# Performance work log

Hardware: AMD Instinct MI355X
Metric: run time of the kernel (lower is better)

## Reference

```python
import jax, jax.numpy as jnp
import numpy as np

B, S, D, H, HS = 4, 2048, 1024, 16, 64
DFF = 4 * D
EPS = 1e-5


def setup_inputs() -> dict:
    key = jax.random.key(0)
    ks = jax.random.split(key, 16)
    std = 0.02
    return {
        "x": jax.random.normal(ks[0], (B, S, D), jnp.float32),
        "Wq": jax.random.normal(ks[1], (H, D, HS), jnp.float32) * std,
        "bq": jnp.zeros((H, HS), jnp.float32),
        "Wk": jax.random.normal(ks[2], (H, D, HS), jnp.float32) * std,
        "bk": jnp.zeros((H, HS), jnp.float32),
        "Wv": jax.random.normal(ks[3], (H, D, HS), jnp.float32) * std,
        "bv": jnp.zeros((H, HS), jnp.float32),
        "Wp": jax.random.normal(ks[4], (D, D), jnp.float32) * std,
        "bp": jnp.zeros((D,), jnp.float32),
        "ln1_w": jnp.ones((D,), jnp.float32),
        "ln1_b": jnp.zeros((D,), jnp.float32),
        "ln2_w": jnp.ones((D,), jnp.float32),
        "ln2_b": jnp.zeros((D,), jnp.float32),
        "W1": jax.random.normal(ks[5], (D, DFF), jnp.float32) * std,
        "b1": jnp.zeros((DFF,), jnp.float32),
        "W2": jax.random.normal(ks[6], (DFF, D), jnp.float32) * std,
        "b2": jnp.zeros((D,), jnp.float32),
    }


def _layernorm(x, w, b):
    mu = jnp.mean(x, axis=-1, keepdims=True)
    var = jnp.mean(jnp.square(x - mu), axis=-1, keepdims=True)
    return (x - mu) * jax.lax.rsqrt(var + EPS) * w + b


def _block(x, Wq, bq, Wk, bk, Wv, bv, Wp, bp, ln1_w, ln1_b, ln2_w, ln2_b, W1, b1, W2, b2):
    seq = x.shape[1]
    xn = _layernorm(x, ln1_w, ln1_b)
    # batched per-head projections: [B,H,S,HS]
    q = jnp.einsum('bsd,hdk->bhsk', xn, Wq) + bq[:, None, :]
    k = jnp.einsum('bsd,hdk->bhsk', xn, Wk) + bk[:, None, :]
    v = jnp.einsum('bsd,hdk->bhsk', xn, Wv) + bv[:, None, :]
    scores = jnp.einsum('bhsk,bhtk->bhst', q, k)
    mask = jnp.tril(jnp.ones((seq, seq), bool))
    # original: masked_fill(-inf) then divide by sqrt(head_size) -> equivalent
    scores = jnp.where(mask, scores / jnp.sqrt(jnp.float32(HS)), -jnp.inf)
    attn = jax.nn.softmax(scores, axis=-1)
    out = jnp.einsum('bhst,bhtk->bhsk', attn, v)
    out = out.transpose(0, 2, 1, 3).reshape(x.shape[0], seq, H * HS)
    att = out @ Wp + bp
    x = x + att
    xn2 = _layernorm(x, ln2_w, ln2_b)
    h = jax.nn.gelu(xn2 @ W1 + b1, approximate=False)  # torch nn.GELU default = exact
    ffn = h @ W2 + b2
    return x + ffn


def reference(x, Wq, bq, Wk, bk, Wv, bv, Wp, bp, ln1_w, ln1_b, ln2_w, ln2_b, W1, b1, W2, b2):
    out = _block(x, Wq, bq, Wk, bk, Wv, bv, Wp, bp, ln1_w, ln1_b, ln2_w, ln2_b, W1, b1, W2, b2)
    return out
```

## Files before the change

### kernel.cpp

```cpp
#include <hip/hip_runtime.h>
#include <hip/hip_bf16.h>

#define D_MODEL 1024
#define SEQ 2048
#define NH 16
#define HSZ 64
#define DFF_ 4096

typedef __attribute__((ext_vector_type(8))) short short8;
typedef __attribute__((ext_vector_type(4))) short short4v;
typedef __attribute__((ext_vector_type(4))) float f32x4;

static __device__ __forceinline__ short f2bf(float f) {
  unsigned u = __builtin_bit_cast(unsigned, f);
  u = u + 0x7fffu + ((u >> 16) & 1u);
  return (short)(u >> 16);
}

static __device__ __forceinline__ unsigned packbf2(float a, float b) {
  return (unsigned)(unsigned short)f2bf(a) | ((unsigned)(unsigned short)f2bf(b) << 16);
}

static __device__ __forceinline__ f32x4 mfma16(short8 a, short8 b, f32x4 c) {
  return __builtin_amdgcn_mfma_f32_16x16x32_bf16(a, b, c, 0, 0, 0);
}

static __device__ __forceinline__ void gld16(const short* g, short* l) {
  __builtin_amdgcn_global_load_lds((const __attribute__((address_space(1))) void*)g,
                                   (__attribute__((address_space(3))) void*)l, 16, 0, 0);
}

#define SM_SCALE 0.18033688011112042f
#define VMW(n) asm volatile("s_waitcnt vmcnt(" #n ")" ::: "memory")

__global__ void transpose_qkv_kernel(const float* __restrict__ Wq, const float* __restrict__ Wk,
                                     const float* __restrict__ Wv, short* __restrict__ dst) {
  __shared__ float tile[32][33];
  const int z = blockIdx.z;
  const int which = z >> 4, hh = z & 15;
  const float* src = (which == 0 ? Wq : which == 1 ? Wk : Wv) + (long)hh * (D_MODEL * HSZ);
  const int c0 = blockIdx.x * 32, r0 = blockIdx.y * 32;
  const int tx = threadIdx.x, ty = threadIdx.y;
#pragma unroll
  for (int i = 0; i < 4; ++i)
    tile[ty + 8 * i][tx] = src[(long)(r0 + ty + 8 * i) * HSZ + c0 + tx];
  __syncthreads();
#pragma unroll
  for (int i = 0; i < 4; ++i)
    dst[((long)which * 1024 + hh * 64 + c0 + ty + 8 * i) * D_MODEL + r0 + tx] =
        f2bf(tile[tx][ty + 8 * i]);
}

__global__ void transpose_gen_kernel(const float* __restrict__ src, short* __restrict__ dst,
                                     int R, int C) {
  __shared__ float tile[32][33];
  const int c0 = blockIdx.x * 32, r0 = blockIdx.y * 32;
  const int tx = threadIdx.x, ty = threadIdx.y;
#pragma unroll
  for (int i = 0; i < 4; ++i)
    tile[ty + 8 * i][tx] = src[(long)(r0 + ty + 8 * i) * C + c0 + tx];
  __syncthreads();
#pragma unroll
  for (int i = 0; i < 4; ++i)
    dst[(long)(c0 + ty + 8 * i) * R + r0 + tx] = f2bf(tile[tx][ty + 8 * i]);
}

__global__ void v_transpose_kernel(const short* __restrict__ vb, short* __restrict__ vt) {
  __shared__ short tile[64 * 72];
  const int bh = blockIdx.y;
  const int t0 = blockIdx.x * 64;
  const long base = (long)bh * SEQ * HSZ;
  const int tid = threadIdx.x;
  const int r = tid >> 3, c = (tid & 7) * 8;
#pragma unroll
  for (int it = 0; it < 2; ++it) {
    const int rr = r + it * 32;
    *(short8*)&tile[rr * 72 + c] = *(const short8*)(vb + base + (long)(t0 + rr) * HSZ + c);
  }
  __syncthreads();
#pragma unroll
  for (int it = 0; it < 2; ++it) {
    const int rr = r + it * 32;
    short8 o;
#pragma unroll
    for (int u = 0; u < 8; ++u) o[u] = tile[(c + u) * 72 + rr];
    *(short8*)(vt + base + (long)rr * SEQ + t0 + c) = o;
  }
}

__global__ void ln_kernel(const float* __restrict__ x, const float* __restrict__ w,
                          const float* __restrict__ b, short* __restrict__ out) {
  const int row = blockIdx.x;
  const float* xr = x + (size_t)row * D_MODEL;
  const int t = threadIdx.x;
  float4 v = *(const float4*)(xr + t * 4);
  float s = v.x + v.y + v.z + v.w;
  float s2 = v.x * v.x + v.y * v.y + v.z * v.z + v.w * v.w;
#pragma unroll
  for (int o = 1; o < 64; o <<= 1) {
    s += __shfl_xor(s, o, 64);
    s2 += __shfl_xor(s2, o, 64);
  }
  __shared__ float ps[8];
  const int lane = t & 63, wid = t >> 6;
  if (lane == 0) { ps[wid] = s; ps[wid + 4] = s2; }
  __syncthreads();
  s = ps[0] + ps[1] + ps[2] + ps[3];
  s2 = ps[4] + ps[5] + ps[6] + ps[7];
  const float mu = s * (1.0f / D_MODEL);
  const float var = s2 * (1.0f / D_MODEL) - mu * mu;
  const float rs = rsqrtf(var + 1e-5f);
  float4 wv = *(const float4*)(w + t * 4);
  float4 bv = *(const float4*)(b + t * 4);
  short4v o4;
  o4[0] = f2bf((v.x - mu) * rs * wv.x + bv.x);
  o4[1] = f2bf((v.y - mu) * rs * wv.y + bv.y);
  o4[2] = f2bf((v.z - mu) * rs * wv.z + bv.z);
  o4[3] = f2bf((v.w - mu) * rs * wv.w + bv.w);
  *(short4v*)(out + (size_t)row * D_MODEL + t * 4) = o4;
}

template <int MODE, int BM>
__global__ __launch_bounds__(512, 2) void gemm_kernel(
    const short* __restrict__ A, const short* __restrict__ Bt, const int K,
    const float* __restrict__ c0, const float* __restrict__ c1,
    const float* __restrict__ c2, const float* __restrict__ res,
    void* __restrict__ o0, void* __restrict__ o1, void* __restrict__ o2) {
  constexpr int NPH = BM / 64;
  constexpr int NA = BM / 64;
  constexpr int NTOT = NA + 4;
  constexpr int PER = NTOT / NPH;
  constexpr int HM = BM / 2;
  __shared__ short As[2][BM * 64];
  __shared__ short Bs[2][256 * 64];
  const long r0 = (long)blockIdx.y * BM;
  const long n0 = (long)blockIdx.x * 256;
  const int tid = threadIdx.x;
  const int lane = tid & 63, wid = tid >> 6;
  const int wm = wid >> 2, wn = wid & 3;
  const int l16 = lane & 15, lg = lane >> 4;

  long offA[NA], offB[4];
#pragma unroll
  for (int i = 0; i < NA; ++i) {
    const int c = tid + i * 512;
    const int lam = c >> 3, s = c & 7;
    const int cch = lam >> 6, rho = lam & 63;
    const int g = cch * 32 + (rho & 31) + ((rho >> 5) ? HM : 0);
    offA[i] = (long)(r0 + g) * K + ((s ^ (lam & 7)) << 3);
  }
#pragma unroll
  for (int i = 0; i < 4; ++i) {
    const int c = tid + i * 512;
    const int row = c >> 3, s = c & 7;
    offB[i] = (long)(n0 + row) * K + ((s ^ (row & 7)) << 3);
  }

  f32x4 acc[2 * NPH][4];
#pragma unroll
  for (int m = 0; m < 2 * NPH; ++m)
#pragma unroll
    for (int n = 0; n < 4; ++n) {
      f32x4 z = {0.f, 0.f, 0.f, 0.f};
      acc[m][n] = z;
    }

  const int x7 = l16 & 7;
  const int sw0 = (lg ^ x7) * 8, sw1 = ((4 + lg) ^ x7) * 8;

#define STG(j, kt, buf)                                                      \
  {                                                                          \
    if ((j) < 4)                                                             \
      gld16(Bt + offB[(j)] + (kt), &Bs[buf][(tid + (j)*512) * 8]);           \
    else                                                                     \
      gld16(A + offA[(j)-4] + (kt), &As[buf][(tid + ((j)-4) * 512) * 8]);    \
  }

#define GPHASE(P, ENDSTMT)                                                   \
  {                                                                          \
    short8 af[2][2];                                                         \
    _Pragma("unroll") for (int mm = 0; mm < 2; ++mm) {                       \
      const int lam = (P)*64 + wm * 32 + mm * 16 + l16;                      \
      af[mm][0] = *(const short8*)&Ap[lam * 64 + sw0];                       \
      af[mm][1] = *(const short8*)&Ap[lam * 64 + sw1];                       \
    }                                                                        \
    if ((P) == 0) {                                                          \
      _Pragma("unroll") for (int n = 0; n < 4; ++n) {                        \
        const int r = (wn * 64 + n * 16 + l16) * 64;                         \
        bf[n][0] = *(const short8*)&Bp[r + sw0];                             \
        bf[n][1] = *(const short8*)&Bp[r + sw1];                             \
      }                                                                      \
    }                                                                        \
    if (st) {                                                                \
      _Pragma("unroll") for (int j = (P)*PER; j < ((P) + 1) * PER; ++j)      \
          STG(j, ktn, nb);                                                   \
    }                                                                        \
    __builtin_amdgcn_s_barrier();                                            \
    asm volatile("s_waitcnt lgkmcnt(0)" ::: "memory");                       \
    __builtin_amdgcn_sched_barrier(0);                                       \
    __builtin_amdgcn_s_setprio(1);                                           \
    _Pragma("unroll") for (int kk = 0; kk < 2; ++kk)                         \
        _Pragma("unroll") for (int mm = 0; mm < 2; ++mm)                     \
        _Pragma("unroll") for (int n = 0; n < 4; ++n) acc[2 * (P) + mm][n] = \
        mfma16(af[mm][kk], bf[n][kk], acc[2 * (P) + mm][n]);                 \
    __builtin_amdgcn_s_setprio(0);                                           \
    ENDSTMT;                                                                 \
    __builtin_amdgcn_s_barrier();                                            \
  }

  const int NT = K >> 6;
#pragma unroll
  for (int j = 0; j < NTOT; ++j) STG(j, 0, 0);
  if constexpr (BM == 256) VMW(3); else VMW(1);
  __builtin_amdgcn_s_barrier();

  for (int t = 0; t < NT; ++t) {
    const int cur = t & 1, nb = cur ^ 1;
    const short* Ap = As[cur];
    const short* Bp = Bs[cur];
    const bool st = (t + 1 < NT);
    const int ktn = (t + 1) << 6;
    short8 bf[4][2];
    if constexpr (BM == 256) {
      GPHASE(0, { if (st) VMW(4); else VMW(2); });
      GPHASE(1, { if (st) VMW(5); else VMW(1); });
      GPHASE(2, { if (st) VMW(6); else VMW(0); });
      GPHASE(3, { if (st) VMW(3); });
    } else {
      GPHASE(0, { if (st) VMW(3); else VMW(0); });
      GPHASE(1, { if (st) VMW(1); });
    }
  }
#undef GPHASE
#undef STG

#pragma unroll
  for (int m = 0; m < 2 * NPH; ++m) {
    const long rowb = r0 + wm * HM + m * 16 + lg * 4;
#pragma unroll
    for (int n = 0; n < 4; ++n) {
      const long col = n0 + wn * 64 + n * 16 + l16;
#pragma unroll
      for (int j = 0; j < 4; ++j) {
        float val = acc[m][n][j];
        const long rr = rowb + j;
        if (MODE == 0) {
          const int c10 = (int)col & 1023;
          const int which = (int)col >> 10;
          const float* bb = which == 0 ? c0 : which == 1 ? c1 : c2;
          short* oo = (short*)(which == 0 ? o0 : which == 1 ? o1 : o2);
          val += bb[c10];
          if (which == 0) val *= SM_SCALE;
          const long bidx = rr >> 11, sidx = rr & 2047;
          const int h = c10 >> 6, hs = c10 & 63;
          oo[(((bidx * NH) + h) * SEQ + sidx) * HSZ + hs] = f2bf(val);
        } else if (MODE == 1) {
          val += c0[col] + res[rr * D_MODEL + col];
          ((float*)o0)[rr * D_MODEL + col] = val;
        } else if (MODE == 2) {
          val += c0[col];
          const float g = 0.5f * val * (1.0f + erff(val * 0.70710678118654752f));
          ((short*)o0)[rr * DFF_ + col] = f2bf(g);
        } else {
          val += c0[col] + res[rr * D_MODEL + col];
          ((float*)o0)[rr * D_MODEL + col] = val;
        }
      }
    }
  }
}

__global__ void attn_kernel(const short* __restrict__ q, const short* __restrict__ k,
                            const short* __restrict__ vt, short* __restrict__ att) {
  const int qt = (SEQ / 128 - 1) - (int)blockIdx.y;
  const int bh = blockIdx.x;
  const int b = bh >> 4, h = bh & 15;
  const int tid = threadIdx.x;
  const int lane = tid & 63, wq = tid >> 6;
  const int l16 = lane & 15, lg = lane >> 4;
  const long base = (long)bh * SEQ * HSZ;

  __shared__ short Ks[64 * 64];
  __shared__ short Vts[64 * 64];
  __shared__ short Ps[4 * 32 * 72];
  short* Psw = &Ps[wq * 32 * 72];

  const int R0 = qt * 128 + wq * 32;

  short8 qf[2][2];
#pragma unroll
  for (int qn = 0; qn < 2; ++qn)
#pragma unroll
    for (int kk = 0; kk < 2; ++kk)
      qf[qn][kk] =
          *(const short8*)(q + base + (long)(R0 + qn * 16 + l16) * HSZ + kk * 32 + lg * 8);

  float m_[2] = {-INFINITY, -INFINITY};
  float l_[2] = {0.f, 0.f};
  f32x4 oacc[2][4];
#pragma unroll
  for (int qn = 0; qn < 2; ++qn)
#pragma unroll
    for (int hf = 0; hf < 4; ++hf) {
      f32x4 z = {0.f, 0.f, 0.f, 0.f};
      oacc[qn][hf] = z;
    }

  const int srow = tid >> 3, wg = tid & 7;
  const int swc = (wg ^ (srow & 7)) * 8;
  const int x7 = l16 & 7;
  const int rc0 = (lg ^ x7) * 8, rc1 = ((4 + lg) ^ x7) * 8;
  const int tend = (qt + 1) * 128;

  for (int t0 = 0; t0 < tend; t0 += 64) {
    __syncthreads();
#pragma unroll
    for (int it = 0; it < 2; ++it) {
      const int r = srow + it * 32;
      const short8 kv = *(const short8*)(k + base + (long)(t0 + r) * HSZ + wg * 8);
      const short8 vv = *(const short8*)(vt + base + (long)r * SEQ + t0 + wg * 8);
      *(short8*)&Ks[r * 64 + swc] = kv;
      *(short8*)&Vts[r * 64 + swc] = vv;
    }
    __syncthreads();

    if (t0 <= R0 + 31) {
      f32x4 sf[4][2];
#pragma unroll
      for (int tt = 0; tt < 4; ++tt)
#pragma unroll
        for (int qn = 0; qn < 2; ++qn) {
          f32x4 z = {0.f, 0.f, 0.f, 0.f};
          sf[tt][qn] = z;
        }
      __builtin_amdgcn_s_setprio(1);
#pragma unroll
      for (int kk = 0; kk < 2; ++kk)
#pragma unroll
        for (int tt = 0; tt < 4; ++tt) {
          short8 kf = *(const short8*)&Ks[(tt * 16 + l16) * 64 + (kk ? rc1 : rc0)];
#pragma unroll
          for (int qn = 0; qn < 2; ++qn) sf[tt][qn] = mfma16(kf, qf[qn][kk], sf[tt][qn]);
        }
      __builtin_amdgcn_s_setprio(0);

      const bool domask = (t0 + 63 > R0);
      if (domask) {
        const int tb = t0 + lg * 4;
#pragma unroll
        for (int tt = 0; tt < 4; ++tt)
#pragma unroll
          for (int qn = 0; qn < 2; ++qn) {
            const int qg = R0 + qn * 16 + l16;
#pragma unroll
            for (int j = 0; j < 4; ++j)
              if (tb + tt * 16 + j > qg) sf[tt][qn][j] = -INFINITY;
          }
      }

      float mx[2];
#pragma unroll
      for (int qn = 0; qn < 2; ++qn) {
        float m0 = sf[0][qn][0];
#pragma unroll
        for (int tt = 0; tt < 4; ++tt)
#pragma unroll
          for (int j = 0; j < 4; ++j) m0 = fmaxf(m0, sf[tt][qn][j]);
        m0 = fmaxf(m0, __shfl_xor(m0, 16, 64));
        m0 = fmaxf(m0, __shfl_xor(m0, 32, 64));
        mx[qn] = m0;
      }
      const int ok = (mx[0] <= m_[0] + 8.f) && (mx[1] <= m_[1] + 8.f);
      if (!__all(ok)) {
#pragma unroll
        for (int qn = 0; qn < 2; ++qn) {
          const float mnew = fmaxf(m_[qn], mx[qn]);
          const float rc = exp2f(m_[qn] - mnew);
          m_[qn] = mnew;
          l_[qn] *= rc;
#pragma unroll
          for (int hf = 0; hf < 4; ++hf)
#pragma unroll
            for (int j = 0; j < 4; ++j) oacc[qn][hf][j] *= rc;
        }
      }
#pragma unroll
      for (int qn = 0; qn < 2; ++qn) {
        float sum = 0.f;
#pragma unroll
        for (int tt = 0; tt < 4; ++tt)
#pragma unroll
          for (int j = 0; j < 4; ++j) {
            const float p = exp2f(sf[tt][qn][j] - m_[qn]);
            sf[tt][qn][j] = p;
            sum += p;
          }
        l_[qn] += sum;
      }

#pragma unroll
      for (int qn = 0; qn < 2; ++qn)
#pragma unroll
        for (int tt = 0; tt < 4; ++tt) {
          const int ro = (qn * 16 + l16) * 72 + tt * 16 + lg * 4;
          *(unsigned*)&Psw[ro] = packbf2(sf[tt][qn][0], sf[tt][qn][1]);
          *(unsigned*)&Psw[ro + 2] = packbf2(sf[tt][qn][2], sf[tt][qn][3]);
        }

      __builtin_amdgcn_s_setprio(1);
#pragma unroll
      for (int kk = 0; kk < 2; ++kk) {
        short8 pa[2];
#pragma unroll
        for (int qn = 0; qn < 2; ++qn)
          pa[qn] = *(const short8*)&Psw[(qn * 16 + l16) * 72 + kk * 32 + lg * 8];
#pragma unroll
        for (int hf = 0; hf < 4; ++hf) {
          short8 vf = *(const short8*)&Vts[(hf * 16 + l16) * 64 + (kk ? rc1 : rc0)];
#pragma unroll
          for (int qn = 0; qn < 2; ++qn)
            oacc[qn][hf] = mfma16(vf, pa[qn], oacc[qn][hf]);
        }
      }
      __builtin_amdgcn_s_setprio(0);
    }
  }

#pragma unroll
  for (int qn = 0; qn < 2; ++qn) {
    float lt = l_[qn];
    lt += __shfl_xor(lt, 16, 64);
    lt += __shfl_xor(lt, 32, 64);
    const float inv = 1.0f / lt;
    const long row = R0 + qn * 16 + l16;
#pragma unroll
    for (int hf = 0; hf < 4; ++hf) {
      short4v o4;
#pragma unroll
      for (int j = 0; j < 4; ++j) o4[j] = f2bf(oacc[qn][hf][j] * inv);
      *(short4v*)(att + ((long)b * SEQ + row) * D_MODEL + h * HSZ + hf * 16 + lg * 4) = o4;
    }
  }
}

extern "C" void kernel_launch(void* const* d_in, const int* in_sizes, int n_in,
                              void* d_out, int out_size, void* d_ws, size_t ws_size,
                              hipStream_t stream) {
  const float* x = (const float*)d_in[0];
  const float* Wq = (const float*)d_in[1];
  const float* bq = (const float*)d_in[2];
  const float* Wk = (const float*)d_in[3];
  const float* bk = (const float*)d_in[4];
  const float* Wv = (const float*)d_in[5];
  const float* bv = (const float*)d_in[6];
  const float* Wp = (const float*)d_in[7];
  const float* bp = (const float*)d_in[8];
  const float* g1 = (const float*)d_in[9];
  const float* be1 = (const float*)d_in[10];
  const float* g2 = (const float*)d_in[11];
  const float* be2 = (const float*)d_in[12];
  const float* W1 = (const float*)d_in[13];
  const float* b1 = (const float*)d_in[14];
  const float* W2 = (const float*)d_in[15];
  const float* b2 = (const float*)d_in[16];
  float* out = (float*)d_out;
  char* ws = (char*)d_ws;

  if (ws_size < 209715200ull) return;

  short* WqkvT = (short*)(ws + 0);
  short* WpT = (short*)(ws + 6291456);
  short* W1T = (short*)(ws + 8388608);
  short* W2T = (short*)(ws + 16777216);
  short* xn = (short*)(ws + 25165824);
  short* vt = (short*)(ws + 25165824);
  short* qb = (short*)(ws + 41943040);
  short* kb = (short*)(ws + 58720256);
  short* vb = (short*)(ws + 75497472);
  short* att = (short*)(ws + 92274688);
  float* x1 = (float*)(ws + 109051904);
  short* hb = (short*)(ws + 142606336);

  dim3 tb(32, 8);
  transpose_qkv_kernel<<<dim3(2, 32, 48), tb, 0, stream>>>(Wq, Wk, Wv, WqkvT);
  transpose_gen_kernel<<<dim3(32, 32), tb, 0, stream>>>(Wp, WpT, 1024, 1024);
  transpose_gen_kernel<<<dim3(128, 32), tb, 0, stream>>>(W1, W1T, 1024, 4096);
  transpose_gen_kernel<<<dim3(32, 128), tb, 0, stream>>>(W2, W2T, 4096, 1024);
  ln_kernel<<<8192, 256, 0, stream>>>(x, g1, be1, xn);
  gemm_kernel<0, 128><<<dim3(12, 64), 512, 0, stream>>>(xn, WqkvT, 1024, bq, bk, bv,
                                                        nullptr, qb, kb, vb);
  v_transpose_kernel<<<dim3(32, 64), 256, 0, stream>>>(vb, vt);
  attn_kernel<<<dim3(64, 16), 256, 0, stream>>>(qb, kb, vt, att);
  gemm_kernel<1, 128><<<dim3(4, 64), 512, 0, stream>>>(att, WpT, 1024, bp, nullptr,
                                                       nullptr, x, x1, nullptr, nullptr);
  ln_kernel<<<8192, 256, 0, stream>>>(x1, g2, be2, xn);
  gemm_kernel<2, 256><<<dim3(16, 32), 512, 0, stream>>>(xn, W1T, 1024, b1, nullptr,
                                                        nullptr, nullptr, hb, nullptr,
                                                        nullptr);
  gemm_kernel<3, 128><<<dim3(4, 64), 512, 0, stream>>>(hb, W2T, 4096, b2, nullptr,
                                                       nullptr, x1, out, nullptr, nullptr);
}
```

Baseline: 414.8 us.

## Add dedicated 256x256 GEMM with 8-phase interleaved staging for QKV and FFN1

Adds a specialized 256x256-tile GEMM kernel that splits each pair of K-tiles into eight phases, each issuing a quarter of the next tile's global-to-LDS loads while running MFMAs, with finer-grained vmcnt waits. The QKV projection moves from 128-row tiles to 256-row tiles (halving grid rows), and the FFN up-projection uses the new kernel. The generic gemm kernel is trimmed to the 128-row residual modes. This aims to improve load/compute overlap and operand reuse; the 256x256 tile uses more LDS and registers, which may limit occupancy, and the smaller QKV grid may underfill the CUs.

```diff
diff --git a/kernel.cpp b/kernel.cpp
--- a/kernel.cpp
+++ b/kernel.cpp
@@ -118,6 +118,153 @@
   o4[2] = f2bf((v.z - mu) * rs * wv.z + bv.z);
   o4[3] = f2bf((v.w - mu) * rs * wv.w + bv.w);
   *(short4v*)(out + (size_t)row * D_MODEL + t * 4) = o4;
+}
+
+template <int MODE>
+__global__ __launch_bounds__(512, 2) void gemm256_kernel(
+    const short* __restrict__ A, const short* __restrict__ Bt, const int K,
+    const float* __restrict__ c0, const float* __restrict__ c1,
+    const float* __restrict__ c2, void* __restrict__ o0, void* __restrict__ o1,
+    void* __restrict__ o2) {
+  __shared__ short As[2][256 * 64];
+  __shared__ short Bs[2][256 * 64];
+  const long r0 = (long)blockIdx.y * 256;
+  const long n0 = (long)blockIdx.x * 256;
+  const int tid = threadIdx.x;
+  const int lane = tid & 63, wid = tid >> 6;
+  const int wm = wid >> 2, wn = wid & 3;
+  const int l16 = lane & 15, lg = lane >> 4;
+
+  long offA[4], offB[4];
+#pragma unroll
+  for (int i = 0; i < 4; ++i) {
+    const int c = tid + i * 512;
+    const int lam = c >> 3, s = c & 7;
+    const int cch = lam >> 6, rho = lam & 63;
+    const int g = cch * 32 + (rho & 31) + ((rho >> 5) ? 128 : 0);
+    offA[i] = (long)(r0 + g) * K + ((s ^ (lam & 7)) << 3);
+    offB[i] = (long)(n0 + lam) * K + ((s ^ (lam & 7)) << 3);
+  }
+
+  f32x4 acc[8][4];
+#pragma unroll
+  for (int m = 0; m < 8; ++m)
+#pragma unroll
+    for (int n = 0; n < 4; ++n) {
+      f32x4 z = {0.f, 0.f, 0.f, 0.f};
+      acc[m][n] = z;
+    }
+
+  const int x7 = l16 & 7;
+  const int sw0 = (lg ^ x7) * 8, sw1 = ((4 + lg) ^ x7) * 8;
+
+#define SA(T, buf, h)                                                          \
+  {                                                                            \
+    gld16(A + offA[2 * (h)] + ((T) << 6), &As[buf][(tid + (2 * (h)) * 512) * 8]); \
+    gld16(A + offA[2 * (h) + 1] + ((T) << 6),                                  \
+          &As[buf][(tid + (2 * (h) + 1) * 512) * 8]);                          \
+  }
+#define SB(T, buf, h)                                                          \
+  {                                                                            \
+    gld16(Bt + offB[2 * (h)] + ((T) << 6), &Bs[buf][(tid + (2 * (h)) * 512) * 8]); \
+    gld16(Bt + offB[2 * (h) + 1] + ((T) << 6),                                 \
+          &Bs[buf][(tid + (2 * (h) + 1) * 512) * 8]);                          \
+  }
+
+#define PH(P, STAGE, WAITST)                                                   \
+  {                                                                            \
+    const short* Ap = As[(P) < 4 ? 0 : 1];                                     \
+    const short* Bp = Bs[(P) < 4 ? 0 : 1];                                     \
+    short8 af[2][2];                                                           \
+    _Pragma("unroll") for (int mm = 0; mm < 2; ++mm) {                         \
+      const int lam = ((P) & 3) * 64 + wm * 32 + mm * 16 + l16;                \
+      af[mm][0] = *(const short8*)&Ap[lam * 64 + sw0];                         \
+      af[mm][1] = *(const short8*)&Ap[lam * 64 + sw1];                         \
+    }                                                                          \
+    if (((P) & 3) == 0) {                                                      \
+      _Pragma("unroll") for (int n = 0; n < 4; ++n) {                          \
+        const int r = (wn * 64 + n * 16 + l16) * 64;                           \
+        bf[n][0] = *(const short8*)&Bp[r + sw0];                               \
+        bf[n][1] = *(const short8*)&Bp[r + sw1];                               \
+      }                                                                        \
+    }                                                                          \
+    STAGE;                                                                     \
+    __builtin_amdgcn_s_barrier();                                              \
+    asm volatile("s_waitcnt lgkmcnt(0)" ::: "memory");                         \
+    __builtin_amdgcn_sched_barrier(0);                                         \
+    __builtin_amdgcn_s_setprio(1);                                             \
+    _Pragma("unroll") for (int kk = 0; kk < 2; ++kk)                           \
+        _Pragma("unroll") for (int mm = 0; mm < 2; ++mm)                       \
+        _Pragma("unroll") for (int n = 0; n < 4; ++n)                          \
+            acc[((P) & 3) * 2 + mm][n] =                                       \
+        mfma16(af[mm][kk], bf[n][kk], acc[((P) & 3) * 2 + mm][n]);             \
+    __builtin_amdgcn_s_setprio(0);                                             \
+    WAITST;                                                                    \
+    __builtin_amdgcn_s_barrier();                                              \
+  }
+
+  const int NT = K >> 6;
+  const int NI = NT >> 1;
+  SB(0, 0, 0); SB(0, 0, 1); SA(0, 0, 0); SA(0, 0, 1);
+  SB(1, 1, 0); SB(1, 1, 1); SA(1, 1, 0);
+  VMW(8);
+  __builtin_amdgcn_s_barrier();
+
+  for (int i = 0; i < NI; ++i) {
+    const int T0 = 2 * i, T1 = 2 * i + 1;
+    short8 bf[4][2];
+    if (i + 1 < NI) {
+      PH(0, SA(T1, 1, 1), ((void)0));
+      PH(1, SB(T0 + 2, 0, 0), VMW(10));
+      PH(2, SB(T0 + 2, 0, 1), ((void)0));
+      PH(3, SA(T0 + 2, 0, 0), VMW(8));
+      PH(4, SA(T0 + 2, 0, 1), ((void)0));
+      PH(5, SB(T1 + 2, 1, 0), VMW(10));
+      PH(6, SB(T1 + 2, 1, 1), ((void)0));
+      PH(7, SA(T1 + 2, 1, 0), VMW(8));
+    } else {
+      PH(0, SA(T1, 1, 1), VMW(0));
+      PH(1, ((void)0), ((void)0));
+      PH(2, ((void)0), ((void)0));
+      PH(3, ((void)0), ((void)0));
+      PH(4, ((void)0), ((void)0));
+      PH(5, ((void)0), ((void)0));
+      PH(6, ((void)0), ((void)0));
+      PH(7, ((void)0), ((void)0));
+    }
+  }
+#undef PH
+#undef SA
+#undef SB
+
+#pragma unroll
+  for (int m = 0; m < 8; ++m) {
+    const long rowb = r0 + wm * 128 + (m >> 1) * 32 + (m & 1) * 16 + lg * 4;
+#pragma unroll
+    for (int n = 0; n < 4; ++n) {
+      const long col = n0 + wn * 64 + n * 16 + l16;
+#pragma unroll
+      for (int j = 0; j < 4; ++j) {
+        float val = acc[m][n][j];
+        const long rr = rowb + j;
+        if (MODE == 0) {
+          const int c10 = (int)col & 1023;
+          const int which = (int)col >> 10;
+          const float* bb = which == 0 ? c0 : which == 1 ? c1 : c2;
+          short* oo = (short*)(which == 0 ? o0 : which == 1 ? o1 : o2);
+          val += bb[c10];
+          if (which == 0) val *= SM_SCALE;
+          const long bidx = rr >> 11, sidx = rr & 2047;
+          const int h = c10 >> 6, hs = c10 & 63;
+          oo[(((bidx * NH) + h) * SEQ + sidx) * HSZ + hs] = f2bf(val);
+        } else {
+          val += c0[col];
+          const float g = 0.5f * val * (1.0f + erff(val * 0.70710678118654752f));
+          ((short*)o0)[rr * DFF_ + col] = f2bf(g);
+        }
+      }
+    }
+  }
 }
 
 template <int MODE, int BM>
@@ -211,7 +358,7 @@
   const int NT = K >> 6;
 #pragma unroll
   for (int j = 0; j < NTOT; ++j) STG(j, 0, 0);
-  if constexpr (BM == 256) VMW(3); else VMW(1);
+  VMW(1);
   __builtin_amdgcn_s_barrier();
 
   for (int t = 0; t < NT; ++t) {
@@ -221,15 +368,8 @@
     const bool st = (t + 1 < NT);
     const int ktn = (t + 1) << 6;
     short8 bf[4][2];
-    if constexpr (BM == 256) {
-      GPHASE(0, { if (st) VMW(4); else VMW(2); });
-      GPHASE(1, { if (st) VMW(5); else VMW(1); });
-      GPHASE(2, { if (st) VMW(6); else VMW(0); });
-      GPHASE(3, { if (st) VMW(3); });
-    } else {
-      GPHASE(0, { if (st) VMW(3); else VMW(0); });
-      GPHASE(1, { if (st) VMW(1); });
-    }
+    GPHASE(0, { if (st) VMW(3); else VMW(0); });
+    GPHASE(1, { if (st) VMW(1); });
   }
 #undef GPHASE
 #undef STG
@@ -244,23 +384,9 @@
       for (int j = 0; j < 4; ++j) {
         float val = acc[m][n][j];
         const long rr = rowb + j;
-        if (MODE == 0) {
-          const int c10 = (int)col & 1023;
-          const int which = (int)col >> 10;
-          const float* bb = which == 0 ? c0 : which == 1 ? c1 : c2;
-          short* oo = (short*)(which == 0 ? o0 : which == 1 ? o1 : o2);
-          val += bb[c10];
-          if (which == 0) val *= SM_SCALE;
-          const long bidx = rr >> 11, sidx = rr & 2047;
-          const int h = c10 >> 6, hs = c10 & 63;
-          oo[(((bidx * NH) + h) * SEQ + sidx) * HSZ + hs] = f2bf(val);
-        } else if (MODE == 1) {
+        if (MODE == 1) {
           val += c0[col] + res[rr * D_MODEL + col];
           ((float*)o0)[rr * D_MODEL + col] = val;
-        } else if (MODE == 2) {
-          val += c0[col];
-          const float g = 0.5f * val * (1.0f + erff(val * 0.70710678118654752f));
-          ((short*)o0)[rr * DFF_ + col] = f2bf(g);
         } else {
           val += c0[col] + res[rr * D_MODEL + col];
           ((float*)o0)[rr * D_MODEL + col] = val;
@@ -487,16 +613,15 @@
   transpose_gen_kernel<<<dim3(128, 32), tb, 0, stream>>>(W1, W1T, 1024, 4096);
   transpose_gen_kernel<<<dim3(32, 128), tb, 0, stream>>>(W2, W2T, 4096, 1024);
   ln_kernel<<<8192, 256, 0, stream>>>(x, g1, be1, xn);
-  gemm_kernel<0, 128><<<dim3(12, 64), 512, 0, stream>>>(xn, WqkvT, 1024, bq, bk, bv,
-                                                        nullptr, qb, kb, vb);
+  gemm256_kernel<0><<<dim3(12, 32), 512, 0, stream>>>(xn, WqkvT, 1024, bq, bk, bv, qb,
+                                                      kb, vb);
   v_transpose_kernel<<<dim3(32, 64), 256, 0, stream>>>(vb, vt);
   attn_kernel<<<dim3(64, 16), 256, 0, stream>>>(qb, kb, vt, att);
   gemm_kernel<1, 128><<<dim3(4, 64), 512, 0, stream>>>(att, WpT, 1024, bp, nullptr,
                                                        nullptr, x, x1, nullptr, nullptr);
   ln_kernel<<<8192, 256, 0, stream>>>(x1, g2, be2, xn);
-  gemm_kernel<2, 256><<<dim3(16, 32), 512, 0, stream>>>(xn, W1T, 1024, b1, nullptr,
-                                                        nullptr, nullptr, hb, nullptr,
-                                                        nullptr);
+  gemm256_kernel<2><<<dim3(16, 32), 512, 0, stream>>>(xn, W1T, 1024, b1, nullptr,
+                                                      nullptr, hb, nullptr, nullptr);
   gemm_kernel<3, 128><<<dim3(4, 64), 512, 0, stream>>>(hb, W2T, 4096, b2, nullptr,
                                                        nullptr, x1, out, nullptr, nullptr);
 }
```

Result: slower. 848.6 us (+104.6%).
